# Kernel optimization log

Hardware: AMD Instinct MI355X
Metric: run time of the kernel (lower is better)

The kernel has to match this reference:

```python
import jax, jax.numpy as jnp
import numpy as np


def setup_inputs() -> dict:
    key = jax.random.key(0)
    k1, k2 = jax.random.split(key)
    B, T, D, K = 16, 4096, 512, 2048
    x = jax.random.normal(k1, (B, T, D), dtype=jnp.float32)
    embed = jax.random.normal(k2, (K, D), dtype=jnp.float32)
    return {"x": x, "embed": embed}


def reference(x, embed):
    # encode: flatten to [N, D], nearest codebook entry by squared L2
    orig_shape = x.shape
    d = orig_shape[-1]
    flat = x.reshape(-1, d)  # [N, D]
    x_sq = jnp.sum(flat * flat, axis=1, keepdims=True)          # [N, 1]
    e_sq = jnp.sum(embed * embed, axis=1)[None, :]               # [1, K]
    dist = -(x_sq - 2.0 * (flat @ embed.T) + e_sq)               # [N, K]
    embed_ind = jnp.argmax(dist, axis=-1)                        # [N]
    embed_ind = embed_ind.reshape(orig_shape[:-1])               # [B, T]
    # decode: embedding gather
    quantize = embed[embed_ind]                                  # [B, T, D]
    return embed_ind, quantize
```

## Files before the change

kernel.cpp:

```cpp
#include <hip/hip_runtime.h>
#include <stdint.h>

#define DIM 512
#define BM  128
#define BK  128
#define DT  32
#define LDSX (BM + 4)

typedef __attribute__((ext_vector_type(8))) _Float16 f16x8;
typedef __attribute__((ext_vector_type(4))) _Float16 f16x4;
typedef __attribute__((ext_vector_type(4))) float f32x4;

__device__ __forceinline__ void async_cp16(const void* g, void* l) {
    __builtin_amdgcn_global_load_lds(
        (const __attribute__((address_space(1))) unsigned int*)g,
        (__attribute__((address_space(3))) unsigned int*)l, 16, 0, 0);
}

__global__ __launch_bounds__(256)
void esq_kernel(const float* __restrict__ embed, float* __restrict__ e_sq, int K) {
    int wave = (blockIdx.x * blockDim.x + threadIdx.x) >> 6;
    int lane = threadIdx.x & 63;
    if (wave >= K) return;
    const float* row = embed + (size_t)wave * DIM;
    float s = 0.f;
#pragma unroll
    for (int j = 0; j < DIM / 64; ++j) { float v = row[lane + 64 * j]; s += v * v; }
#pragma unroll
    for (int off = 32; off; off >>= 1) s += __shfl_down(s, off, 64);
    if (lane == 0) e_sq[wave] = s;
}

__global__ __launch_bounds__(256)
void cvt_f16_kernel(const float* __restrict__ src, _Float16* __restrict__ dst, int n4) {
    int i = blockIdx.x * 256 + threadIdx.x;
    if (i >= n4) return;
    float4 v = ((const float4*)src)[i];
    f16x4 h;
    h[0] = (_Float16)v.x; h[1] = (_Float16)v.y; h[2] = (_Float16)v.z; h[3] = (_Float16)v.w;
    ((f16x4*)dst)[i] = h;
}

template<int GV>
__device__ __forceinline__ void compute_group(const _Float16* ebuf,
    const f16x8 (&ah)[2][16], f32x4 (&acc)[2][4], int quad, int l15)
{
#pragma unroll
    for (int dtl = 0; dtl < 4; ++dtl) {
#pragma unroll
        for (int kwi = 0; kwi < 2; ++kwi) {
            const int pch = (kwi * 4 + quad) ^ (l15 & 7);
            f16x8 bh[4];
#pragma unroll
            for (int nt = 0; nt < 4; ++nt)
                bh[nt] = *(const f16x8*)(ebuf + dtl * 4096 + (nt * 16 + l15) * 64 + pch * 8);
#pragma unroll
            for (int mt = 0; mt < 2; ++mt)
#pragma unroll
                for (int nt = 0; nt < 4; ++nt)
                    acc[mt][nt] = __builtin_amdgcn_mfma_f32_16x16x32_f16(
                        ah[mt][(GV * 4 + dtl) * 2 + kwi], bh[nt], acc[mt][nt], 0, 0, 0);
        }
    }
}

__global__ __launch_bounds__(256, 2)
void vq_reg_kernel(const float* __restrict__ x, const _Float16* __restrict__ eh,
                   const float* __restrict__ e_sq, int* __restrict__ cand)
{
    __shared__ __align__(16) char smem[73728];
    _Float16* EB = (_Float16*)smem;
    const float* esq_l = (const float*)(smem + 65536);
    uint32_t* rk = (uint32_t*)smem;

    const int tid  = threadIdx.x;
    const int w    = tid >> 6, lane = tid & 63;
    const int quad = lane >> 4, l15 = lane & 15;
    const int r0   = blockIdx.x * 128;
    const int wrow = r0 + w * 32;

    uint32_t goff[8];
#pragma unroll
    for (int i = 0; i < 8; ++i) {
        const int s   = w * 512 + i * 64 + lane;
        const int dtl = s >> 9;
        const int rr  = (s >> 3) & 63;
        const int lch = (s & 7) ^ (rr & 7);
        goff[i] = (uint32_t)(rr * 512 + dtl * 64 + lch * 8);
    }

#pragma unroll
    for (int i = 0; i < 2; ++i) {
        const int sb = w * 128 + i * 64;
        async_cp16(e_sq + (size_t)(sb + lane) * 4, smem + 65536 + sb * 16);
    }
#pragma unroll
    for (int i = 0; i < 8; ++i)
        async_cp16(eh + goff[i], smem + (w * 512 + i * 64) * 16);

    f16x8 ah[2][16];
#pragma unroll
    for (int mt = 0; mt < 2; ++mt) {
        const float* xr = x + (size_t)(wrow + mt * 16 + l15) * DIM + quad * 8;
#pragma unroll
        for (int kw = 0; kw < 16; ++kw) {
            const float4 a0 = *(const float4*)(xr + kw * 32);
            const float4 a1 = *(const float4*)(xr + kw * 32 + 4);
            f16x8 h;
            h[0] = (_Float16)a0.x; h[1] = (_Float16)a0.y;
            h[2] = (_Float16)a0.z; h[3] = (_Float16)a0.w;
            h[4] = (_Float16)a1.x; h[5] = (_Float16)a1.y;
            h[6] = (_Float16)a1.z; h[7] = (_Float16)a1.w;
            ah[mt][kw] = h;
        }
    }

    uint32_t b1[8], b2[8];
#pragma unroll
    for (int i = 0; i < 8; ++i) { b1[i] = 0xFFFFFFFFu; b2[i] = 0xFFFFFFFFu; }

    __syncthreads();

    for (int kt = 0; kt < 32; ++kt) {
        f32x4 acc[2][4];
#pragma unroll
        for (int mt = 0; mt < 2; ++mt)
#pragma unroll
            for (int nt = 0; nt < 4; ++nt)
#pragma unroll
                for (int r = 0; r < 4; ++r) acc[mt][nt][r] = 0.f;

        const size_t kb = (size_t)kt * 32768;

#pragma unroll
        for (int i = 0; i < 8; ++i)
            async_cp16(eh + kb + 256 + goff[i], smem + 32768 + (w * 512 + i * 64) * 16);
        compute_group<0>(EB, ah, acc, quad, l15);
        __syncthreads();

        if (kt + 1 < 32) {
#pragma unroll
            for (int i = 0; i < 8; ++i)
                async_cp16(eh + kb + 32768 + goff[i], smem + (w * 512 + i * 64) * 16);
        }
        compute_group<1>(EB + 16384, ah, acc, quad, l15);
        __syncthreads();

#pragma unroll
        for (int nt = 0; nt < 4; ++nt) {
            const int c = kt * 64 + nt * 16 + l15;
            const float eqb = esq_l[c] + 1024.0f;
#pragma unroll
            for (int mt = 0; mt < 2; ++mt)
#pragma unroll
                for (int r = 0; r < 4; ++r) {
                    const float v = fmaf(-2.0f, acc[mt][nt][r], eqb);
                    const uint32_t u = (__float_as_uint(v) & 0xFFFFF800u) | (uint32_t)c;
                    const int s = mt * 4 + r;
                    const uint32_t mx = u > b1[s] ? u : b1[s];
                    b2[s] = mx < b2[s] ? mx : b2[s];
                    b1[s] = u < b1[s] ? u : b1[s];
                }
        }
    }

#pragma unroll
    for (int mt = 0; mt < 2; ++mt)
#pragma unroll
        for (int r = 0; r < 4; ++r) {
            const int row = w * 32 + mt * 16 + quad * 4 + r;
            const int s = mt * 4 + r;
            rk[row * 33 + l15 * 2]     = b1[s];
            rk[row * 33 + l15 * 2 + 1] = b2[s];
        }
    __syncthreads();
    if (tid < 128) {
        uint32_t t0 = 0xFFFFFFFFu, t1 = t0, t2 = t0, t3 = t0;
        for (int e = 0; e < 32; ++e) {
            const uint32_t u = rk[tid * 33 + e];
            if (u < t3) {
                if (u < t0)      { t3 = t2; t2 = t1; t1 = t0; t0 = u; }
                else if (u < t1) { t3 = t2; t2 = t1; t1 = u; }
                else if (u < t2) { t3 = t2; t2 = u; }
                else               t3 = u;
            }
        }
        const float v0 = __uint_as_float(t0 & 0xFFFFF800u);
        const float v1 = __uint_as_float(t1 & 0xFFFFF800u);
        uint32_t c0 = t0 & 2047u;
        if (!(v1 - v0 >= 1.0f)) c0 |= 0x80000000u;
        int4 c4;
        c4.x = (int)c0;
        c4.y = (int)(t1 & 2047u);
        c4.z = (int)(t2 & 2047u);
        c4.w = (int)(t3 & 2047u);
        *(int4*)(cand + (size_t)(r0 + tid) * 4) = c4;
    }
}

__global__ __launch_bounds__(256)
void verify_gather4_kernel(const float* __restrict__ x, const float* __restrict__ embed,
                           const float* __restrict__ e_sq, const int* __restrict__ cand,
                           float* __restrict__ out_idx, float* __restrict__ out_q) {
    const int row  = blockIdx.x * 4 + (threadIdx.x >> 6);
    const int lane = threadIdx.x & 63;
    const int4 cc = *(const int4*)(cand + (size_t)row * 4);
    f32x4* oq = (f32x4*)(out_q + (size_t)row * DIM);
    if (cc.x >= 0) {
        const f32x4* er = (const f32x4*)(embed + (size_t)cc.x * DIM);
        const f32x4 e0 = er[lane];
        const f32x4 e1 = er[lane + 64];
        oq[lane]      = e0;
        oq[lane + 64] = e1;
        if (lane == 0) out_idx[row] = (float)cc.x;
    } else {
        const f32x4* xr = (const f32x4*)(x + (size_t)row * DIM);
        const f32x4 xv0 = xr[lane];
        const f32x4 xv1 = xr[lane + 64];
        const int cs[4] = {cc.x & 2047, cc.y & 2047, cc.z & 2047, cc.w & 2047};
        float best = 3.4e38f;
        int   bi   = 0x7fffffff;
        f32x4 g0 = {0.f, 0.f, 0.f, 0.f}, g1 = {0.f, 0.f, 0.f, 0.f};
#pragma unroll
        for (int k = 0; k < 4; ++k) {
            const int c = cs[k];
            const f32x4* er = (const f32x4*)(embed + (size_t)c * DIM);
            const f32x4 e0 = er[lane];
            const f32x4 e1 = er[lane + 64];
            float d = xv0[0] * e0[0] + xv0[1] * e0[1] + xv0[2] * e0[2] + xv0[3] * e0[3]
                    + xv1[0] * e1[0] + xv1[1] * e1[1] + xv1[2] * e1[2] + xv1[3] * e1[3];
#pragma unroll
            for (int off = 32; off; off >>= 1) d += __shfl_xor(d, off, 64);
            const float s = e_sq[c] - 2.0f * d;
            const bool better = (s < best) || (s == best && c < bi);
            best = better ? s : best;
            bi   = better ? c : bi;
            g0 = better ? e0 : g0;
            g1 = better ? e1 : g1;
        }
        if (lane == 0) out_idx[row] = (float)bi;
        oq[lane]      = g0;
        oq[lane + 64] = g1;
    }
}

__global__ __launch_bounds__(256)
void vq_argmin_kernel(const float* __restrict__ x, const float* __restrict__ embed,
                      const float* __restrict__ e_sq, float* __restrict__ out_idx,
                      int N, int K) {
    __shared__ float xs[DT * LDSX];
    __shared__ float es[DT * LDSX];
    __shared__ float sval[BM * 17];
    __shared__ int   sidx[BM * 17];
    const int tid = threadIdx.x;
    const int tx = tid & 15, ty = tid >> 4;
    const int r0 = blockIdx.x * BM;
    float best_val[8]; int best_idx[8];
#pragma unroll
    for (int i = 0; i < 8; ++i) { best_val[i] = 3.4e38f; best_idx[i] = 0; }
    const int nkt = K / BK;
    for (int kt = 0; kt < nkt; ++kt) {
        float acc[8][8];
#pragma unroll
        for (int i = 0; i < 8; ++i)
#pragma unroll
            for (int j = 0; j < 8; ++j) acc[i][j] = 0.f;
        for (int dt = 0; dt < DIM / DT; ++dt) {
            __syncthreads();
#pragma unroll
            for (int k = 0; k < 4; ++k) {
                int l = tid + k * 256, row = l >> 3, q = l & 7;
                const float4 v = *(const float4*)(x + (size_t)(r0 + row) * DIM + dt * DT + q * 4);
                xs[(q * 4 + 0) * LDSX + row] = v.x; xs[(q * 4 + 1) * LDSX + row] = v.y;
                xs[(q * 4 + 2) * LDSX + row] = v.z; xs[(q * 4 + 3) * LDSX + row] = v.w;
            }
#pragma unroll
            for (int k = 0; k < 4; ++k) {
                int l = tid + k * 256, row = l >> 3, q = l & 7;
                const float4 v = *(const float4*)(embed + (size_t)(kt * BK + row) * DIM + dt * DT + q * 4);
                es[(q * 4 + 0) * LDSX + row] = v.x; es[(q * 4 + 1) * LDSX + row] = v.y;
                es[(q * 4 + 2) * LDSX + row] = v.z; es[(q * 4 + 3) * LDSX + row] = v.w;
            }
            __syncthreads();
#pragma unroll
            for (int d = 0; d < DT; ++d) {
                const float4 a0 = *(const float4*)&xs[d * LDSX + 4 * ty];
                const float4 a1 = *(const float4*)&xs[d * LDSX + 4 * ty + 64];
                const float4 b0 = *(const float4*)&es[d * LDSX + 4 * tx];
                const float4 b1 = *(const float4*)&es[d * LDSX + 4 * tx + 64];
                const float a[8] = {a0.x, a0.y, a0.z, a0.w, a1.x, a1.y, a1.z, a1.w};
                const float b[8] = {b0.x, b0.y, b0.z, b0.w, b1.x, b1.y, b1.z, b1.w};
#pragma unroll
                for (int i = 0; i < 8; ++i)
#pragma unroll
                    for (int j = 0; j < 8; ++j) acc[i][j] += a[i] * b[j];
            }
        }
#pragma unroll
        for (int j = 0; j < 8; ++j) {
            const int c = kt * BK + 4 * tx + (j & 3) + 64 * (j >> 2);
            const float eq = e_sq[c];
#pragma unroll
            for (int i = 0; i < 8; ++i) {
                const float s = eq - 2.0f * acc[i][j];
                if (s < best_val[i]) { best_val[i] = s; best_idx[i] = c; }
            }
        }
    }
    __syncthreads();
#pragma unroll
    for (int i = 0; i < 8; ++i) {
        const int r = 4 * ty + (i & 3) + 64 * (i >> 2);
        sval[r * 17 + tx] = best_val[i]; sidx[r * 17 + tx] = best_idx[i];
    }
    __syncthreads();
    if (tid < BM) {
        float bv = sval[tid * 17 + 0]; int bi = sidx[tid * 17 + 0];
#pragma unroll
        for (int t = 1; t < 16; ++t) {
            const float v = sval[tid * 17 + t]; const int ix = sidx[tid * 17 + t];
            if (v < bv || (v == bv && ix < bi)) { bv = v; bi = ix; }
        }
        out_idx[r0 + tid] = (float)bi;
    }
}

__global__ __launch_bounds__(256)
void gather_kernel(const float* __restrict__ embed, const float* __restrict__ idx_f,
                   float* __restrict__ out_q) {
    const int row = blockIdx.x * 2 + (threadIdx.x >> 7);
    const int c = threadIdx.x & 127;
    const int idx = (int)idx_f[row];
    const float4 v = *(const float4*)(embed + (size_t)idx * DIM + c * 4);
    *(float4*)(out_q + (size_t)row * DIM + c * 4) = v;
}

extern "C" void kernel_launch(void* const* d_in, const int* in_sizes, int n_in,
                              void* d_out, int out_size, void* d_ws, size_t ws_size,
                              hipStream_t stream) {
    const float* x     = (const float*)d_in[0];
    const float* embed = (const float*)d_in[1];
    const int N = in_sizes[0] / DIM;
    const int K = in_sizes[1] / DIM;

    float* out_idx = (float*)d_out;
    float* out_q   = (float*)d_out + N;
    char* ws = (char*)d_ws;

    const size_t off_cand = 8192;
    const size_t off_eh   = off_cand + (size_t)N * 16;
    const size_t need     = off_eh + (size_t)K * DIM * 2;

    float* e_sq = (float*)ws;
    esq_kernel<<<(K + 3) / 4, 256, 0, stream>>>(embed, e_sq, K);

    if (ws_size >= need && K == 2048 && (N % 128) == 0) {
        _Float16* eh = (_Float16*)(ws + off_eh);
        int* cand = (int*)(ws + off_cand);
        cvt_f16_kernel<<<(K * DIM / 4 + 255) / 256, 256, 0, stream>>>(embed, eh, K * DIM / 4);
        vq_reg_kernel<<<N / 128, 256, 0, stream>>>(x, eh, e_sq, cand);
        verify_gather4_kernel<<<N / 4, 256, 0, stream>>>(x, embed, e_sq, cand, out_idx, out_q);
    } else {
        vq_argmin_kernel<<<N / BM, 256, 0, stream>>>(x, embed, e_sq, out_idx, N, K);
        gather_kernel<<<N / 2, 256, 0, stream>>>(embed, out_idx, out_q);
    }
}
```

Baseline: 363.9 us.

## Fuse candidate verification and embedding gather into the fp16 MFMA search kernel

Result: no change. 358.3 us (-1.5%).

```diff
diff --git a/kernel.cpp b/kernel.cpp
--- a/kernel.cpp
+++ b/kernel.cpp
@@ -65,13 +65,15 @@
 }
 
 __global__ __launch_bounds__(256, 2)
-void vq_reg_kernel(const float* __restrict__ x, const _Float16* __restrict__ eh,
-                   const float* __restrict__ e_sq, int* __restrict__ cand)
+void vq_fused_kernel(const float* __restrict__ x, const float* __restrict__ embed,
+                     const _Float16* __restrict__ eh, const float* __restrict__ e_sq,
+                     float* __restrict__ out_idx, float* __restrict__ out_q)
 {
     __shared__ __align__(16) char smem[73728];
     _Float16* EB = (_Float16*)smem;
     const float* esq_l = (const float*)(smem + 65536);
     uint32_t* rk = (uint32_t*)smem;
+    uint32_t* cl = (uint32_t*)(smem + 32768);
 
     const int tid  = threadIdx.x;
     const int w    = tid >> 6, lane = tid & 63;
@@ -189,58 +191,53 @@
         const float v1 = __uint_as_float(t1 & 0xFFFFF800u);
         uint32_t c0 = t0 & 2047u;
         if (!(v1 - v0 >= 1.0f)) c0 |= 0x80000000u;
-        int4 c4;
-        c4.x = (int)c0;
-        c4.y = (int)(t1 & 2047u);
-        c4.z = (int)(t2 & 2047u);
-        c4.w = (int)(t3 & 2047u);
-        *(int4*)(cand + (size_t)(r0 + tid) * 4) = c4;
-    }
-}
-
-__global__ __launch_bounds__(256)
-void verify_gather4_kernel(const float* __restrict__ x, const float* __restrict__ embed,
-                           const float* __restrict__ e_sq, const int* __restrict__ cand,
-                           float* __restrict__ out_idx, float* __restrict__ out_q) {
-    const int row  = blockIdx.x * 4 + (threadIdx.x >> 6);
-    const int lane = threadIdx.x & 63;
-    const int4 cc = *(const int4*)(cand + (size_t)row * 4);
-    f32x4* oq = (f32x4*)(out_q + (size_t)row * DIM);
-    if (cc.x >= 0) {
-        const f32x4* er = (const f32x4*)(embed + (size_t)cc.x * DIM);
-        const f32x4 e0 = er[lane];
-        const f32x4 e1 = er[lane + 64];
-        oq[lane]      = e0;
-        oq[lane + 64] = e1;
-        if (lane == 0) out_idx[row] = (float)cc.x;
-    } else {
-        const f32x4* xr = (const f32x4*)(x + (size_t)row * DIM);
-        const f32x4 xv0 = xr[lane];
-        const f32x4 xv1 = xr[lane + 64];
-        const int cs[4] = {cc.x & 2047, cc.y & 2047, cc.z & 2047, cc.w & 2047};
-        float best = 3.4e38f;
-        int   bi   = 0x7fffffff;
-        f32x4 g0 = {0.f, 0.f, 0.f, 0.f}, g1 = {0.f, 0.f, 0.f, 0.f};
-#pragma unroll
-        for (int k = 0; k < 4; ++k) {
-            const int c = cs[k];
-            const f32x4* er = (const f32x4*)(embed + (size_t)c * DIM);
+        cl[tid * 4 + 0] = c0;
+        cl[tid * 4 + 1] = t1 & 2047u;
+        cl[tid * 4 + 2] = t2 & 2047u;
+        cl[tid * 4 + 3] = t3 & 2047u;
+    }
+    __syncthreads();
+
+    for (int i = 0; i < 32; ++i) {
+        const int row  = wrow + i;
+        const int lrow = w * 32 + i;
+        const uint32_t c0 = cl[lrow * 4 + 0];
+        f32x4* oq = (f32x4*)(out_q + (size_t)row * DIM);
+        if (!(c0 & 0x80000000u)) {
+            const f32x4* er = (const f32x4*)(embed + (size_t)c0 * DIM);
             const f32x4 e0 = er[lane];
             const f32x4 e1 = er[lane + 64];
-            float d = xv0[0] * e0[0] + xv0[1] * e0[1] + xv0[2] * e0[2] + xv0[3] * e0[3]
-                    + xv1[0] * e1[0] + xv1[1] * e1[1] + xv1[2] * e1[2] + xv1[3] * e1[3];
-#pragma unroll
-            for (int off = 32; off; off >>= 1) d += __shfl_xor(d, off, 64);
-            const float s = e_sq[c] - 2.0f * d;
-            const bool better = (s < best) || (s == best && c < bi);
-            best = better ? s : best;
-            bi   = better ? c : bi;
-            g0 = better ? e0 : g0;
-            g1 = better ? e1 : g1;
-        }
-        if (lane == 0) out_idx[row] = (float)bi;
-        oq[lane]      = g0;
-        oq[lane + 64] = g1;
+            oq[lane]      = e0;
+            oq[lane + 64] = e1;
+            if (lane == 0) out_idx[row] = (float)c0;
+        } else {
+            const f32x4* xr = (const f32x4*)(x + (size_t)row * DIM);
+            const f32x4 xv0 = xr[lane];
+            const f32x4 xv1 = xr[lane + 64];
+            float best = 3.4e38f;
+            int   bi   = 0x7fffffff;
+            f32x4 g0 = {0.f, 0.f, 0.f, 0.f}, g1 = {0.f, 0.f, 0.f, 0.f};
+#pragma unroll
+            for (int k = 0; k < 4; ++k) {
+                const int c = (int)(cl[lrow * 4 + k] & 2047u);
+                const f32x4* er = (const f32x4*)(embed + (size_t)c * DIM);
+                const f32x4 e0 = er[lane];
+                const f32x4 e1 = er[lane + 64];
+                float d = xv0[0] * e0[0] + xv0[1] * e0[1] + xv0[2] * e0[2] + xv0[3] * e0[3]
+                        + xv1[0] * e1[0] + xv1[1] * e1[1] + xv1[2] * e1[2] + xv1[3] * e1[3];
+#pragma unroll
+                for (int off = 32; off; off >>= 1) d += __shfl_xor(d, off, 64);
+                const float s = esq_l[c] - 2.0f * d;
+                const bool better = (s < best) || (s == best && c < bi);
+                best = better ? s : best;
+                bi   = better ? c : bi;
+                g0 = better ? e0 : g0;
+                g1 = better ? e1 : g1;
+            }
+            if (lane == 0) out_idx[row] = (float)bi;
+            oq[lane]      = g0;
+            oq[lane + 64] = g1;
+        }
     }
 }
 
@@ -347,19 +344,16 @@
     float* out_q   = (float*)d_out + N;
     char* ws = (char*)d_ws;
 
-    const size_t off_cand = 8192;
-    const size_t off_eh   = off_cand + (size_t)N * 16;
-    const size_t need     = off_eh + (size_t)K * DIM * 2;
+    const size_t off_eh = 8192;
+    const size_t need   = off_eh + (size_t)K * DIM * 2;
 
     float* e_sq = (float*)ws;
     esq_kernel<<<(K + 3) / 4, 256, 0, stream>>>(embed, e_sq, K);
 
     if (ws_size >= need && K == 2048 && (N % 128) == 0) {
         _Float16* eh = (_Float16*)(ws + off_eh);
-        int* cand = (int*)(ws + off_cand);
         cvt_f16_kernel<<<(K * DIM / 4 + 255) / 256, 256, 0, stream>>>(embed, eh, K * DIM / 4);
-        vq_reg_kernel<<<N / 128, 256, 0, stream>>>(x, eh, e_sq, cand);
-        verify_gather4_kernel<<<N / 4, 256, 0, stream>>>(x, embed, e_sq, cand, out_idx, out_q);
+        vq_fused_kernel<<<N / 128, 256, 0, stream>>>(x, embed, eh, e_sq, out_idx, out_q);
     } else {
         vq_argmin_kernel<<<N / BM, 256, 0, stream>>>(x, embed, e_sq, out_idx, N, K);
         gather_kernel<<<N / 2, 256, 0, stream>>>(embed, out_idx, out_q);
```
